# Kernel optimization log

Measured on AMD Instinct MI355X. Metric: run time of the kernel, lower is better.

Reference implementation:

```python
import jax, jax.numpy as jnp
import numpy as np

N, D, E = 50000, 128, 800000


def setup_inputs() -> dict:
    key = jax.random.key(0)
    ks = jax.random.split(key, 12)
    s = 1.0 / np.sqrt(D)
    return {
        "x": jax.random.normal(ks[0], (N, D), jnp.float32),
        "edge_index": jax.random.randint(ks[1], (2, E), 0, N, jnp.int32),
        "W1": jax.random.normal(ks[2], (D, D), jnp.float32) * s,
        "bc1": jnp.zeros((D,), jnp.float32),
        "W2": jax.random.normal(ks[3], (D, D), jnp.float32) * s,
        "bc2": jnp.zeros((D,), jnp.float32),
        "w11": jax.random.normal(ks[4], (D, D), jnp.float32) * s,
        "w12": jax.random.normal(ks[5], (D, D), jnp.float32) * s,
        "b1": jax.random.uniform(ks[6], (D,), jnp.float32, -s, s),
        "w21": jax.random.normal(ks[7], (D, D), jnp.float32) * s,
        "w22": jax.random.normal(ks[8], (D, D), jnp.float32) * s,
        "b2": jax.random.uniform(ks[9], (D,), jnp.float32, -s, s),
    }


def gcn_conv(x, W, b, src, dst):
    """PyG GCNConv: self-loops + symmetric D^-1/2 (A+I) D^-1/2 normalization."""
    n = x.shape[0]
    h = x @ W  # [N, D]
    ones = jnp.ones(dst.shape[0], h.dtype)
    deg = jax.ops.segment_sum(ones, dst, num_segments=n) + 1.0  # +1 for self-loop
    dinv = jax.lax.rsqrt(deg)
    norm = dinv[src] * dinv[dst]  # [E]
    agg = jax.ops.segment_sum(h[src] * norm[:, None], dst, num_segments=n)
    agg = agg + h * (dinv * dinv)[:, None]  # self-loop messages
    return agg + b


def reference(x, edge_index, W1, bc1, W2, bc2, w11, w12, b1, w21, w22, b2):
    src, dst = edge_index[0], edge_index[1]
    # layer 1: forward and reversed edge directions (dropout is identity in eval)
    o1 = jax.nn.relu(gcn_conv(x, W1, bc1, src, dst))
    o2 = jax.nn.relu(gcn_conv(x, W1, bc1, dst, src))
    G = jax.nn.sigmoid(o1 @ w11.T + o2 @ w12.T + b1)
    h = G * o1 + (1.0 - G) * o2
    # layer 2
    p1 = jax.nn.relu(gcn_conv(h, W2, bc2, src, dst))
    p2 = jax.nn.relu(gcn_conv(h, W2, bc2, dst, src))
    G2 = jax.nn.sigmoid(p1 @ w21.T + p2 @ w22.T + b2)
    return G2 * p1 + (1.0 - G2) * p2
```

## Files before the change

kernel.cpp:

```cpp
#include <hip/hip_runtime.h>
#include <hip/hip_bf16.h>
#include <hip/hip_fp16.h>
#include <math.h>

#define D 128
#define SEG 4096
#define BSH 7
#define RCAP 4096
#define ACAP 4096
#define TRS 133

typedef _Float16 half8  __attribute__((ext_vector_type(8)));
typedef _Float16 half4v __attribute__((ext_vector_type(4)));
typedef float    fx4    __attribute__((ext_vector_type(4)));

__global__ __launch_bounds__(256) void scat2_kernel(const int* __restrict__ src,
                                                    const int* __restrict__ dst,
                                                    int e, int nb,
                                                    int* __restrict__ gcur1, int* __restrict__ gcur2,
                                                    unsigned int* __restrict__ rec1,
                                                    unsigned int* __restrict__ rec2) {
    __shared__ int h1[512], h2[512], o1[512], o2[512], run1[512], run2[512];
    int tid = threadIdx.x;
    for (int b = tid; b < nb; b += 256) { h1[b] = 0; h2[b] = 0; run1[b] = 0; run2[b] = 0; }
    __syncthreads();
    int s0 = blockIdx.x * SEG;
    int s1 = min(e, s0 + SEG);
    for (int idx = s0 + tid; idx < s1; idx += 256) {
        atomicAdd(&h1[dst[idx] >> BSH], 1);
        atomicAdd(&h2[src[idx] >> BSH], 1);
    }
    __syncthreads();
    for (int b = tid; b < nb; b += 256) {
        o1[b] = atomicAdd(&gcur1[b], h1[b]);
        o2[b] = atomicAdd(&gcur2[b], h2[b]);
    }
    __syncthreads();
    for (int idx = s0 + tid; idx < s1; idx += 256) {
        unsigned int sv = (unsigned int)src[idx];
        unsigned int dv = (unsigned int)dst[idx];
        int b1 = dv >> BSH, b2 = sv >> BSH;
        int p1 = o1[b1] + atomicAdd(&run1[b1], 1);
        if (p1 < RCAP) rec1[(size_t)b1 * RCAP + p1] = (dv << 16) | sv;
        int p2 = o2[b2] + atomicAdd(&run2[b2], 1);
        if (p2 < RCAP) rec2[(size_t)b2 * RCAP + p2] = (sv << 16) | dv;
    }
}

__global__ __launch_bounds__(256) void fin_kernel(const unsigned int* __restrict__ rec1,
                                                  const unsigned int* __restrict__ rec2,
                                                  const int* __restrict__ gcur1, const int* __restrict__ gcur2,
                                                  unsigned short* __restrict__ adj1, unsigned short* __restrict__ adj2,
                                                  int* __restrict__ ip1, int* __restrict__ ipe1,
                                                  int* __restrict__ ip2, int* __restrict__ ipe2,
                                                  float* __restrict__ dinv1, float* __restrict__ dinv2,
                                                  int n) {
    __shared__ unsigned int Lrec[RCAP];
    __shared__ unsigned short sadj[ACAP];
    __shared__ int deg[128], pscan[128], cur[128];
    __shared__ int ptot_s;
    int bkt = blockIdx.x;
    int dir = blockIdx.y;
    const unsigned int* rec = dir ? rec2 : rec1;
    const int* gc = dir ? gcur2 : gcur1;
    unsigned short* adj = dir ? adj2 : adj1;
    int* ip  = dir ? ip2 : ip1;
    int* ipe = dir ? ipe2 : ipe1;
    float* dinv = dir ? dinv2 : dinv1;

    int tid = threadIdx.x;
    int cnt = gc[bkt];
    if (cnt > RCAP) cnt = RCAP;
    size_t rbase = (size_t)bkt * RCAP;
    if (tid < 128) { deg[tid] = 0; cur[tid] = 0; }
    for (int i = tid; i < cnt; i += 256) Lrec[i] = rec[rbase + i];
    __syncthreads();
    int base = bkt << BSH;
    for (int i = tid; i < cnt; i += 256)
        atomicAdd(&deg[(int)(Lrec[i] >> 16) - base], 1);
    __syncthreads();
    if (tid < 128) pscan[tid] = (deg[tid] + 7) & ~7;
    __syncthreads();
    #pragma unroll
    for (int st = 1; st < 128; st <<= 1) {
        int add = (tid < 128 && tid >= st) ? pscan[tid - st] : 0;
        __syncthreads();
        if (tid < 128) pscan[tid] += add;
        __syncthreads();
    }
    if (tid == 127) ptot_s = min(pscan[127], ACAP);
    __syncthreads();
    int ptot = ptot_s;
    for (int i = tid; i < ptot; i += 256) sadj[i] = (unsigned short)n;
    __syncthreads();
    for (int i = tid; i < cnt; i += 256) {
        unsigned int r = Lrec[i];
        int l = (int)(r >> 16) - base;
        int pd = (deg[l] + 7) & ~7;
        int pos = pscan[l] - pd + atomicAdd(&cur[l], 1);
        if (pos < ACAP) sadj[pos] = (unsigned short)(r & 0xffffu);
    }
    __syncthreads();
    int gbase = bkt * ACAP;
    for (int i = tid; i < ptot; i += 256) adj[gbase + i] = sadj[i];
    if (tid < 128) {
        int node = base + tid;
        if (node < n) {
            int pd = (deg[tid] + 7) & ~7;
            ip[node]  = gbase + pscan[tid] - pd;
            ipe[node] = gbase + pscan[tid];
            dinv[node] = rsqrtf((float)deg[tid] + 1.0f);
        }
    }
    if (bkt == 0 && tid == 200) dinv[n] = 0.0f;
}

__global__ __launch_bounds__(256) void prep_kernel(const float* __restrict__ W1, const float* __restrict__ W2,
                                                   const float* __restrict__ w11, const float* __restrict__ w12,
                                                   const float* __restrict__ w21, const float* __restrict__ w22,
                                                   _Float16* __restrict__ T1, _Float16* __restrict__ T2,
                                                   _Float16* __restrict__ o11, _Float16* __restrict__ o12,
                                                   _Float16* __restrict__ o21, _Float16* __restrict__ o22) {
    __shared__ float s[32][33];
    int which = blockIdx.y;
    if (which < 2) {
        const float* w = which ? W2 : W1;
        _Float16* t = which ? T2 : T1;
        int tk = (blockIdx.x >> 2) * 32;
        int tc = (blockIdx.x & 3) * 32;
        int lr = threadIdx.x >> 5;
        int lc = threadIdx.x & 31;
        #pragma unroll
        for (int i = 0; i < 32; i += 8)
            s[lr + i][lc] = w[(size_t)(tk + lr + i) * D + tc + lc];
        __syncthreads();
        #pragma unroll
        for (int i = 0; i < 32; i += 8)
            t[(size_t)(tc + lr + i) * D + tk + lc] = (_Float16)s[lc][lr + i];
    } else {
        int wsel = which - 2;
        const float* w = (wsel == 0) ? w11 : (wsel == 1) ? w12 : (wsel == 2) ? w21 : w22;
        _Float16* o = (wsel == 0) ? o11 : (wsel == 1) ? o12 : (wsel == 2) ? o21 : o22;
        int idx = (blockIdx.x * 256 + threadIdx.x) * 4;
        float4 v = *(const float4*)&w[idx];
        half4v h = {(_Float16)v.x, (_Float16)v.y, (_Float16)v.z, (_Float16)v.w};
        *(half4v*)&o[idx] = h;
    }
}

__global__ __launch_bounds__(256) void gemm_f32a_kernel(const float* __restrict__ A,
                                                        const _Float16* __restrict__ Wt,
                                                        _Float16* __restrict__ C16, int n) {
    __shared__ float trs[4][16 * TRS];
    int tid = threadIdx.x;
    int wv = tid >> 6, lane = tid & 63;
    int m = lane & 15, q = lane >> 4;
    int row0 = blockIdx.x * 128 + wv * 32;
    size_t ar0 = (size_t)min(row0 + m, n - 1) * D;
    size_t ar1 = (size_t)min(row0 + 16 + m, n - 1) * D;
    fx4 acc[2][8];
    #pragma unroll
    for (int t = 0; t < 2; t++)
        #pragma unroll
        for (int ct = 0; ct < 8; ct++) acc[t][ct] = (fx4){0.f, 0.f, 0.f, 0.f};
    #pragma unroll
    for (int ks = 0; ks < 4; ks++) {
        int k0 = ks * 32 + q * 8;
        half8 bf[8];
        #pragma unroll
        for (int ct = 0; ct < 8; ct++)
            bf[ct] = *(const half8*)&Wt[(size_t)(ct * 16 + m) * D + k0];
        float4 u0 = *(const float4*)&A[ar0 + k0];
        float4 u1 = *(const float4*)&A[ar0 + k0 + 4];
        half8 a0 = {(_Float16)u0.x, (_Float16)u0.y, (_Float16)u0.z, (_Float16)u0.w,
                    (_Float16)u1.x, (_Float16)u1.y, (_Float16)u1.z, (_Float16)u1.w};
        float4 v0 = *(const float4*)&A[ar1 + k0];
        float4 v1 = *(const float4*)&A[ar1 + k0 + 4];
        half8 a1 = {(_Float16)v0.x, (_Float16)v0.y, (_Float16)v0.z, (_Float16)v0.w,
                    (_Float16)v1.x, (_Float16)v1.y, (_Float16)v1.z, (_Float16)v1.w};
        #pragma unroll
        for (int ct = 0; ct < 8; ct++) {
            acc[0][ct] = __builtin_amdgcn_mfma_f32_16x16x32_f16(a0, bf[ct], acc[0][ct], 0, 0, 0);
            acc[1][ct] = __builtin_amdgcn_mfma_f32_16x16x32_f16(a1, bf[ct], acc[1][ct], 0, 0, 0);
        }
    }
    float* Wl = trs[wv];
    #pragma unroll
    for (int t = 0; t < 2; t++) {
        #pragma unroll
        for (int reg = 0; reg < 4; reg++)
            #pragma unroll
            for (int ct = 0; ct < 8; ct++)
                Wl[(q * 4 + reg) * TRS + ct * 16 + m] = acc[t][ct][reg];
        int r = row0 + t * 16 + m;
        if (r < n) {
            size_t rr = (size_t)r * D;
            #pragma unroll
            for (int ks = 0; ks < 4; ks++) {
                int c0 = ks * 32 + q * 8;
                float4 p0 = *(const float4*)&Wl[m * TRS + c0];
                float4 p1 = *(const float4*)&Wl[m * TRS + c0 + 4];
                half8 hv = {(_Float16)p0.x, (_Float16)p0.y, (_Float16)p0.z, (_Float16)p0.w,
                            (_Float16)p1.x, (_Float16)p1.y, (_Float16)p1.z, (_Float16)p1.w};
                *(half8*)&C16[rr + c0] = hv;
            }
        }
    }
}

__global__ __launch_bounds__(256) void gemm_f16a_kernel(const _Float16* __restrict__ A,
                                                        const _Float16* __restrict__ Wt,
                                                        _Float16* __restrict__ C16, int n) {
    __shared__ float trs[4][16 * TRS];
    int tid = threadIdx.x;
    int wv = tid >> 6, lane = tid & 63;
    int m = lane & 15, q = lane >> 4;
    int row0 = blockIdx.x * 128 + wv * 32;
    size_t ar0 = (size_t)min(row0 + m, n - 1) * D;
    size_t ar1 = (size_t)min(row0 + 16 + m, n - 1) * D;
    fx4 acc[2][8];
    #pragma unroll
    for (int t = 0; t < 2; t++)
        #pragma unroll
        for (int ct = 0; ct < 8; ct++) acc[t][ct] = (fx4){0.f, 0.f, 0.f, 0.f};
    #pragma unroll
    for (int ks = 0; ks < 4; ks++) {
        int k0 = ks * 32 + q * 8;
        half8 bf[8];
        #pragma unroll
        for (int ct = 0; ct < 8; ct++)
            bf[ct] = *(const half8*)&Wt[(size_t)(ct * 16 + m) * D + k0];
        half8 a0 = *(const half8*)&A[ar0 + k0];
        half8 a1 = *(const half8*)&A[ar1 + k0];
        #pragma unroll
        for (int ct = 0; ct < 8; ct++) {
            acc[0][ct] = __builtin_amdgcn_mfma_f32_16x16x32_f16(a0, bf[ct], acc[0][ct], 0, 0, 0);
            acc[1][ct] = __builtin_amdgcn_mfma_f32_16x16x32_f16(a1, bf[ct], acc[1][ct], 0, 0, 0);
        }
    }
    float* Wl = trs[wv];
    #pragma unroll
    for (int t = 0; t < 2; t++) {
        #pragma unroll
        for (int reg = 0; reg < 4; reg++)
            #pragma unroll
            for (int ct = 0; ct < 8; ct++)
                Wl[(q * 4 + reg) * TRS + ct * 16 + m] = acc[t][ct][reg];
        int r = row0 + t * 16 + m;
        if (r < n) {
            size_t rr = (size_t)r * D;
            #pragma unroll
            for (int ks = 0; ks < 4; ks++) {
                int c0 = ks * 32 + q * 8;
                float4 p0 = *(const float4*)&Wl[m * TRS + c0];
                float4 p1 = *(const float4*)&Wl[m * TRS + c0 + 4];
                half8 hv = {(_Float16)p0.x, (_Float16)p0.y, (_Float16)p0.z, (_Float16)p0.w,
                            (_Float16)p1.x, (_Float16)p1.y, (_Float16)p1.z, (_Float16)p1.w};
                *(half8*)&C16[rr + c0] = hv;
            }
        }
    }
}

__global__ __launch_bounds__(256) void aggregate2_kernel(const __half* __restrict__ h16,
                                                         const int* __restrict__ ip1,
                                                         const int* __restrict__ ipe1,
                                                         const unsigned short* __restrict__ adj1,
                                                         const float* __restrict__ dinv1,
                                                         const int* __restrict__ ip2,
                                                         const int* __restrict__ ipe2,
                                                         const unsigned short* __restrict__ adj2,
                                                         const float* __restrict__ dinv2,
                                                         const float* __restrict__ bias,
                                                         _Float16* __restrict__ out1,
                                                         _Float16* __restrict__ out2, int n) {
    const int* ip  = blockIdx.y ? ip2 : ip1;
    const int* ipe = blockIdx.y ? ipe2 : ipe1;
    const unsigned short* adj = blockIdx.y ? adj2 : adj1;
    const float* dinv = blockIdx.y ? dinv2 : dinv1;
    _Float16* out = blockIdx.y ? out2 : out1;
    int wid = threadIdx.x >> 6, lane = threadIdx.x & 63;
    int half = lane >> 5, l32 = lane & 31;
    int i = blockIdx.x * 4 + wid;
    if (i >= n) return;
    int beg = ip[i], endp = ipe[i];
    int sh = half * 16;
    float4 acc = make_float4(0.f, 0.f, 0.f, 0.f);
    for (int j = beg; j < endp; j += 8) {
        uint4 av = *(const uint4*)&adj[j];
        int s0 = (av.x >> sh) & 0xffff;
        int s1 = (av.y >> sh) & 0xffff;
        int s2 = (av.z >> sh) & 0xffff;
        int s3 = (av.w >> sh) & 0xffff;
        float w0 = dinv[s0], w1 = dinv[s1], w2 = dinv[s2], w3 = dinv[s3];
        uint2 r0 = *(const uint2*)&h16[(size_t)s0 * D + 4 * l32];
        uint2 r1 = *(const uint2*)&h16[(size_t)s1 * D + 4 * l32];
        uint2 r2 = *(const uint2*)&h16[(size_t)s2 * D + 4 * l32];
        uint2 r3 = *(const uint2*)&h16[(size_t)s3 * D + 4 * l32];
        float2 a0 = __half22float2(*(__half2*)&r0.x), b0 = __half22float2(*(__half2*)&r0.y);
        float2 a1 = __half22float2(*(__half2*)&r1.x), b1 = __half22float2(*(__half2*)&r1.y);
        float2 a2 = __half22float2(*(__half2*)&r2.x), b2 = __half22float2(*(__half2*)&r2.y);
        float2 a3 = __half22float2(*(__half2*)&r3.x), b3 = __half22float2(*(__half2*)&r3.y);
        acc.x += w0 * a0.x + w1 * a1.x + w2 * a2.x + w3 * a3.x;
        acc.y += w0 * a0.y + w1 * a1.y + w2 * a2.y + w3 * a3.y;
        acc.z += w0 * b0.x + w1 * b1.x + w2 * b2.x + w3 * b3.x;
        acc.w += w0 * b0.y + w1 * b1.y + w2 * b2.y + w3 * b3.y;
    }
    acc.x += __shfl_xor(acc.x, 32, 64);
    acc.y += __shfl_xor(acc.y, 32, 64);
    acc.z += __shfl_xor(acc.z, 32, 64);
    acc.w += __shfl_xor(acc.w, 32, 64);
    if (half == 0) {
        float di = dinv[i];
        float d2 = di * di;
        uint2 rs = *(const uint2*)&h16[(size_t)i * D + 4 * l32];
        float2 s0 = __half22float2(*(__half2*)&rs.x);
        float2 s1 = __half22float2(*(__half2*)&rs.y);
        float4 bv = *(const float4*)&bias[4 * l32];
        half4v o;
        o[0] = (_Float16)fmaxf(di * acc.x + d2 * s0.x + bv.x, 0.f);
        o[1] = (_Float16)fmaxf(di * acc.y + d2 * s0.y + bv.y, 0.f);
        o[2] = (_Float16)fmaxf(di * acc.z + d2 * s1.x + bv.z, 0.f);
        o[3] = (_Float16)fmaxf(di * acc.w + d2 * s1.y + bv.w, 0.f);
        *(half4v*)&out[(size_t)i * D + 4 * l32] = o;
    }
}

__global__ __launch_bounds__(256) void gate_mfma_kernel(const _Float16* __restrict__ o1,
                                                        const _Float16* __restrict__ o2,
                                                        const _Float16* __restrict__ w1,
                                                        const _Float16* __restrict__ w2,
                                                        const float* __restrict__ b,
                                                        float* __restrict__ out32,
                                                        _Float16* __restrict__ out16,
                                                        int write16, int n) {
    __shared__ float trs[4][16 * TRS];
    int tid = threadIdx.x;
    int wv = tid >> 6, lane = tid & 63;
    int m = lane & 15, q = lane >> 4;
    int row0 = blockIdx.x * 128 + wv * 32;
    size_t ar0 = (size_t)min(row0 + m, n - 1) * D;
    size_t ar1 = (size_t)min(row0 + 16 + m, n - 1) * D;
    fx4 acc[2][8];
    #pragma unroll
    for (int t = 0; t < 2; t++)
        #pragma unroll
        for (int ct = 0; ct < 8; ct++) acc[t][ct] = (fx4){0.f, 0.f, 0.f, 0.f};
    #pragma unroll
    for (int ks = 0; ks < 4; ks++) {
        int k0 = ks * 32 + q * 8;
        half8 bf1[8], bf2[8];
        #pragma unroll
        for (int ct = 0; ct < 8; ct++) {
            bf1[ct] = *(const half8*)&w1[(size_t)(ct * 16 + m) * D + k0];
            bf2[ct] = *(const half8*)&w2[(size_t)(ct * 16 + m) * D + k0];
        }
        half8 a10 = *(const half8*)&o1[ar0 + k0];
        half8 a20 = *(const half8*)&o2[ar0 + k0];
        half8 a11 = *(const half8*)&o1[ar1 + k0];
        half8 a21 = *(const half8*)&o2[ar1 + k0];
        #pragma unroll
        for (int ct = 0; ct < 8; ct++) {
            acc[0][ct] = __builtin_amdgcn_mfma_f32_16x16x32_f16(a10, bf1[ct], acc[0][ct], 0, 0, 0);
            acc[0][ct] = __builtin_amdgcn_mfma_f32_16x16x32_f16(a20, bf2[ct], acc[0][ct], 0, 0, 0);
            acc[1][ct] = __builtin_amdgcn_mfma_f32_16x16x32_f16(a11, bf1[ct], acc[1][ct], 0, 0, 0);
            acc[1][ct] = __builtin_amdgcn_mfma_f32_16x16x32_f16(a21, bf2[ct], acc[1][ct], 0, 0, 0);
        }
    }
    float bb[4][8];
    #pragma unroll
    for (int ks = 0; ks < 4; ks++) {
        float4 b0 = *(const float4*)&b[ks * 32 + q * 8];
        float4 b1 = *(const float4*)&b[ks * 32 + q * 8 + 4];
        bb[ks][0] = b0.x; bb[ks][1] = b0.y; bb[ks][2] = b0.z; bb[ks][3] = b0.w;
        bb[ks][4] = b1.x; bb[ks][5] = b1.y; bb[ks][6] = b1.z; bb[ks][7] = b1.w;
    }
    float* Wl = trs[wv];
    #pragma unroll
    for (int t = 0; t < 2; t++) {
        #pragma unroll
        for (int reg = 0; reg < 4; reg++)
            #pragma unroll
            for (int ct = 0; ct < 8; ct++)
                Wl[(q * 4 + reg) * TRS + ct * 16 + m] = acc[t][ct][reg];
        int r = row0 + t * 16 + m;
        size_t rr = (size_t)min(r, n - 1) * D;
        #pragma unroll
        for (int ks = 0; ks < 4; ks++) {
            int c0 = ks * 32 + q * 8;
            float4 p0 = *(const float4*)&Wl[m * TRS + c0];
            float4 p1 = *(const float4*)&Wl[m * TRS + c0 + 4];
            half8 u1 = *(const half8*)&o1[rr + c0];
            half8 u2 = *(const half8*)&o2[rr + c0];
            float pv[8] = {p0.x, p0.y, p0.z, p0.w, p1.x, p1.y, p1.z, p1.w};
            float res[8];
            #pragma unroll
            for (int j = 0; j < 8; j++) {
                float tv = pv[j] + bb[ks][j];
                float g = 1.0f / (1.0f + __expf(-tv));
                res[j] = g * (float)u1[j] + (1.0f - g) * (float)u2[j];
            }
            if (r < n) {
                if (write16) {
                    half8 hv = {(_Float16)res[0], (_Float16)res[1], (_Float16)res[2], (_Float16)res[3],
                                (_Float16)res[4], (_Float16)res[5], (_Float16)res[6], (_Float16)res[7]};
                    *(half8*)&out16[rr + c0] = hv;
                } else {
                    *(float4*)&out32[rr + c0]     = make_float4(res[0], res[1], res[2], res[3]);
                    *(float4*)&out32[rr + c0 + 4] = make_float4(res[4], res[5], res[6], res[7]);
                }
            }
        }
    }
}

extern "C" void kernel_launch(void* const* d_in, const int* in_sizes, int n_in,
                              void* d_out, int out_size, void* d_ws, size_t ws_size,
                              hipStream_t stream) {
    const float* x   = (const float*)d_in[0];
    const int*   eix = (const int*)d_in[1];
    const float* W1  = (const float*)d_in[2];
    const float* bc1 = (const float*)d_in[3];
    const float* W2  = (const float*)d_in[4];
    const float* bc2 = (const float*)d_in[5];
    const float* w11 = (const float*)d_in[6];
    const float* w12 = (const float*)d_in[7];
    const float* b1  = (const float*)d_in[8];
    const float* w21 = (const float*)d_in[9];
    const float* w22 = (const float*)d_in[10];
    const float* b2  = (const float*)d_in[11];
    int n = in_sizes[0] / D;
    int e = in_sizes[1] / 2;
    const int* src = eix;
    const int* dst = eix + e;

    int nb = (n + 127) >> BSH;
    int nblk = (e + SEG - 1) / SEG;

    char* p = (char*)d_ws;
    auto alloc = [&](size_t bytes) {
        char* q = p;
        p += (bytes + 255) & ~(size_t)255;
        return q;
    };
    int* gcur1 = (int*)alloc((size_t)2 * 512 * sizeof(int));
    int* gcur2 = gcur1 + 512;
    unsigned int* rec1 = (unsigned int*)alloc((size_t)nb * RCAP * sizeof(unsigned int));
    unsigned int* rec2 = (unsigned int*)alloc((size_t)nb * RCAP * sizeof(unsigned int));
    int*   ip1   = (int*)alloc((size_t)n * sizeof(int));
    int*   ipe1  = (int*)alloc((size_t)n * sizeof(int));
    int*   ip2   = (int*)alloc((size_t)n * sizeof(int));
    int*   ipe2  = (int*)alloc((size_t)n * sizeof(int));
    float* dinv1 = (float*)alloc((size_t)(n + 1) * sizeof(float));
    float* dinv2 = (float*)alloc((size_t)(n + 1) * sizeof(float));
    unsigned short* adj1 = (unsigned short*)alloc((size_t)nb * ACAP * sizeof(unsigned short));
    unsigned short* adj2 = (unsigned short*)alloc((size_t)nb * ACAP * sizeof(unsigned short));
    _Float16* W1t  = (_Float16*)alloc((size_t)D * D * sizeof(_Float16));
    _Float16* W2t  = (_Float16*)alloc((size_t)D * D * sizeof(_Float16));
    _Float16* w11h = (_Float16*)alloc((size_t)D * D * sizeof(_Float16));
    _Float16* w12h = (_Float16*)alloc((size_t)D * D * sizeof(_Float16));
    _Float16* w21h = (_Float16*)alloc((size_t)D * D * sizeof(_Float16));
    _Float16* w22h = (_Float16*)alloc((size_t)D * D * sizeof(_Float16));
    _Float16* h16  = (_Float16*)alloc((size_t)(n + 1) * D * sizeof(_Float16));
    _Float16* o1h  = (_Float16*)alloc((size_t)n * D * sizeof(_Float16));
    _Float16* o2h  = (_Float16*)alloc((size_t)n * D * sizeof(_Float16));
    _Float16* h2h  = (_Float16*)alloc((size_t)n * D * sizeof(_Float16));
    float* outF  = (float*)d_out;

    hipMemsetAsync(gcur1, 0, (size_t)2 * 512 * sizeof(int), stream);
    prep_kernel<<<dim3(16, 6), 256, 0, stream>>>(W1, W2, w11, w12, w21, w22,
                                                 W1t, W2t, w11h, w12h, w21h, w22h);
    scat2_kernel<<<nblk, 256, 0, stream>>>(src, dst, e, nb, gcur1, gcur2, rec1, rec2);
    fin_kernel<<<dim3(nb, 2), 256, 0, stream>>>(rec1, rec2, gcur1, gcur2,
                                                adj1, adj2, ip1, ipe1, ip2, ipe2, dinv1, dinv2, n);

    int gG = (n + 127) / 128;
    int gA = (n + 3) / 4;
    gemm_f32a_kernel<<<gG, 256, 0, stream>>>(x, W1t, h16, n);
    aggregate2_kernel<<<dim3(gA, 2), 256, 0, stream>>>((const __half*)h16,
                                                       ip1, ipe1, adj1, dinv1,
                                                       ip2, ipe2, adj2, dinv2,
                                                       bc1, o1h, o2h, n);
    gate_mfma_kernel<<<gG, 256, 0, stream>>>(o1h, o2h, w11h, w12h, b1,
                                             nullptr, h2h, 1, n);
    gemm_f16a_kernel<<<gG, 256, 0, stream>>>(h2h, W2t, h16, n);
    aggregate2_kernel<<<dim3(gA, 2), 256, 0, stream>>>((const __half*)h16,
                                                       ip1, ipe1, adj1, dinv1,
                                                       ip2, ipe2, adj2, dinv2,
                                                       bc2, o1h, o2h, n);
    gate_mfma_kernel<<<gG, 256, 0, stream>>>(o1h, o2h, w21h, w22h, b2,
                                             outF, nullptr, 0, n);
}
```

Baseline: 330.6 us.

## Pre-scale GEMM outputs by source dinv to drop per-edge degree gathers

The GEMM epilogues now write two fp16 copies of h, each pre-multiplied by the per-node dinv of one edge direction. This lets the aggregation kernel skip the per-edge dinv gather and multiply, and fold the self-loop term as di*(acc + hs[i]). The aggregate loop also prefetches the next adjacency chunk, uses a 32-bit index calculation, and splits the epilogue across both half-waves. The cost is double the GEMM write traffic and an extra N×D fp16 buffer, and the padding row is now zeroed by memset instead of through dinv[n]=0.

```diff
diff --git a/kernel.cpp b/kernel.cpp
--- a/kernel.cpp
+++ b/kernel.cpp
@@ -112,7 +112,6 @@
             dinv[node] = rsqrtf((float)deg[tid] + 1.0f);
         }
     }
-    if (bkt == 0 && tid == 200) dinv[n] = 0.0f;
 }
 
 __global__ __launch_bounds__(256) void prep_kernel(const float* __restrict__ W1, const float* __restrict__ W2,
@@ -150,7 +149,10 @@
 
 __global__ __launch_bounds__(256) void gemm_f32a_kernel(const float* __restrict__ A,
                                                         const _Float16* __restrict__ Wt,
-                                                        _Float16* __restrict__ C16, int n) {
+                                                        const float* __restrict__ dinv1,
+                                                        const float* __restrict__ dinv2,
+                                                        _Float16* __restrict__ hs1,
+                                                        _Float16* __restrict__ hs2, int n) {
     __shared__ float trs[4][16 * TRS];
     int tid = threadIdx.x;
     int wv = tid >> 6, lane = tid & 63;
@@ -194,15 +196,22 @@
                 Wl[(q * 4 + reg) * TRS + ct * 16 + m] = acc[t][ct][reg];
         int r = row0 + t * 16 + m;
         if (r < n) {
+            float s1 = dinv1[r], s2 = dinv2[r];
             size_t rr = (size_t)r * D;
             #pragma unroll
             for (int ks = 0; ks < 4; ks++) {
                 int c0 = ks * 32 + q * 8;
                 float4 p0 = *(const float4*)&Wl[m * TRS + c0];
                 float4 p1 = *(const float4*)&Wl[m * TRS + c0 + 4];
-                half8 hv = {(_Float16)p0.x, (_Float16)p0.y, (_Float16)p0.z, (_Float16)p0.w,
-                            (_Float16)p1.x, (_Float16)p1.y, (_Float16)p1.z, (_Float16)p1.w};
-                *(half8*)&C16[rr + c0] = hv;
+                float pv[8] = {p0.x, p0.y, p0.z, p0.w, p1.x, p1.y, p1.z, p1.w};
+                half8 h1v, h2v;
+                #pragma unroll
+                for (int j = 0; j < 8; j++) {
+                    h1v[j] = (_Float16)(s1 * pv[j]);
+                    h2v[j] = (_Float16)(s2 * pv[j]);
+                }
+                *(half8*)&hs1[rr + c0] = h1v;
+                *(half8*)&hs2[rr + c0] = h2v;
             }
         }
     }
@@ -210,7 +219,10 @@
 
 __global__ __launch_bounds__(256) void gemm_f16a_kernel(const _Float16* __restrict__ A,
                                                         const _Float16* __restrict__ Wt,
-                                                        _Float16* __restrict__ C16, int n) {
+                                                        const float* __restrict__ dinv1,
+                                                        const float* __restrict__ dinv2,
+                                                        _Float16* __restrict__ hs1,
+                                                        _Float16* __restrict__ hs2, int n) {
     __shared__ float trs[4][16 * TRS];
     int tid = threadIdx.x;
     int wv = tid >> 6, lane = tid & 63;
@@ -248,21 +260,29 @@
                 Wl[(q * 4 + reg) * TRS + ct * 16 + m] = acc[t][ct][reg];
         int r = row0 + t * 16 + m;
         if (r < n) {
+            float s1 = dinv1[r], s2 = dinv2[r];
             size_t rr = (size_t)r * D;
             #pragma unroll
             for (int ks = 0; ks < 4; ks++) {
                 int c0 = ks * 32 + q * 8;
                 float4 p0 = *(const float4*)&Wl[m * TRS + c0];
                 float4 p1 = *(const float4*)&Wl[m * TRS + c0 + 4];
-                half8 hv = {(_Float16)p0.x, (_Float16)p0.y, (_Float16)p0.z, (_Float16)p0.w,
-                            (_Float16)p1.x, (_Float16)p1.y, (_Float16)p1.z, (_Float16)p1.w};
-                *(half8*)&C16[rr + c0] = hv;
+                float pv[8] = {p0.x, p0.y, p0.z, p0.w, p1.x, p1.y, p1.z, p1.w};
+                half8 h1v, h2v;
+                #pragma unroll
+                for (int j = 0; j < 8; j++) {
+                    h1v[j] = (_Float16)(s1 * pv[j]);
+                    h2v[j] = (_Float16)(s2 * pv[j]);
+                }
+                *(half8*)&hs1[rr + c0] = h1v;
+                *(half8*)&hs2[rr + c0] = h2v;
             }
         }
     }
 }
 
-__global__ __launch_bounds__(256) void aggregate2_kernel(const __half* __restrict__ h16,
+__global__ __launch_bounds__(256) void aggregate2_kernel(const __half* __restrict__ hs1g,
+                                                         const __half* __restrict__ hs2g,
                                                          const int* __restrict__ ip1,
                                                          const int* __restrict__ ipe1,
                                                          const unsigned short* __restrict__ adj1,
@@ -274,56 +294,60 @@
                                                          const float* __restrict__ bias,
                                                          _Float16* __restrict__ out1,
                                                          _Float16* __restrict__ out2, int n) {
+    const __half* hs = blockIdx.y ? hs2g : hs1g;
     const int* ip  = blockIdx.y ? ip2 : ip1;
     const int* ipe = blockIdx.y ? ipe2 : ipe1;
     const unsigned short* adj = blockIdx.y ? adj2 : adj1;
     const float* dinv = blockIdx.y ? dinv2 : dinv1;
     _Float16* out = blockIdx.y ? out2 : out1;
     int wid = threadIdx.x >> 6, lane = threadIdx.x & 63;
-    int half = lane >> 5, l32 = lane & 31;
+    int hf = lane >> 5, l32 = lane & 31;
     int i = blockIdx.x * 4 + wid;
     if (i >= n) return;
     int beg = ip[i], endp = ipe[i];
-    int sh = half * 16;
+    int fcol = 4 * l32;
     float4 acc = make_float4(0.f, 0.f, 0.f, 0.f);
-    for (int j = beg; j < endp; j += 8) {
-        uint4 av = *(const uint4*)&adj[j];
-        int s0 = (av.x >> sh) & 0xffff;
-        int s1 = (av.y >> sh) & 0xffff;
-        int s2 = (av.z >> sh) & 0xffff;
-        int s3 = (av.w >> sh) & 0xffff;
-        float w0 = dinv[s0], w1 = dinv[s1], w2 = dinv[s2], w3 = dinv[s3];
-        uint2 r0 = *(const uint2*)&h16[(size_t)s0 * D + 4 * l32];
-        uint2 r1 = *(const uint2*)&h16[(size_t)s1 * D + 4 * l32];
-        uint2 r2 = *(const uint2*)&h16[(size_t)s2 * D + 4 * l32];
-        uint2 r3 = *(const uint2*)&h16[(size_t)s3 * D + 4 * l32];
-        float2 a0 = __half22float2(*(__half2*)&r0.x), b0 = __half22float2(*(__half2*)&r0.y);
-        float2 a1 = __half22float2(*(__half2*)&r1.x), b1 = __half22float2(*(__half2*)&r1.y);
-        float2 a2 = __half22float2(*(__half2*)&r2.x), b2 = __half22float2(*(__half2*)&r2.y);
-        float2 a3 = __half22float2(*(__half2*)&r3.x), b3 = __half22float2(*(__half2*)&r3.y);
-        acc.x += w0 * a0.x + w1 * a1.x + w2 * a2.x + w3 * a3.x;
-        acc.y += w0 * a0.y + w1 * a1.y + w2 * a2.y + w3 * a3.y;
-        acc.z += w0 * b0.x + w1 * b1.x + w2 * b2.x + w3 * b3.x;
-        acc.w += w0 * b0.y + w1 * b1.y + w2 * b2.y + w3 * b3.y;
+    if (beg < endp) {
+        int hoff = hf << 2;
+        int j = beg;
+        uint2 iv = *(const uint2*)&adj[j + hoff];
+        while (true) {
+            int jn = j + 8;
+            int jp = jn < endp ? jn : j;
+            uint2 niv = *(const uint2*)&adj[jp + hoff];
+            int s0 = iv.x & 0xffff, s1 = iv.x >> 16;
+            int s2 = iv.y & 0xffff, s3 = iv.y >> 16;
+            uint2 r0 = *(const uint2*)&hs[(s0 << 7) + fcol];
+            uint2 r1 = *(const uint2*)&hs[(s1 << 7) + fcol];
+            uint2 r2 = *(const uint2*)&hs[(s2 << 7) + fcol];
+            uint2 r3 = *(const uint2*)&hs[(s3 << 7) + fcol];
+            float2 a0 = __half22float2(*(__half2*)&r0.x), b0 = __half22float2(*(__half2*)&r0.y);
+            float2 a1 = __half22float2(*(__half2*)&r1.x), b1 = __half22float2(*(__half2*)&r1.y);
+            float2 a2 = __half22float2(*(__half2*)&r2.x), b2 = __half22float2(*(__half2*)&r2.y);
+            float2 a3 = __half22float2(*(__half2*)&r3.x), b3 = __half22float2(*(__half2*)&r3.y);
+            acc.x += a0.x + a1.x + a2.x + a3.x;
+            acc.y += a0.y + a1.y + a2.y + a3.y;
+            acc.z += b0.x + b1.x + b2.x + b3.x;
+            acc.w += b0.y + b1.y + b2.y + b3.y;
+            if (jn >= endp) break;
+            iv = niv; j = jn;
+        }
     }
     acc.x += __shfl_xor(acc.x, 32, 64);
     acc.y += __shfl_xor(acc.y, 32, 64);
     acc.z += __shfl_xor(acc.z, 32, 64);
     acc.w += __shfl_xor(acc.w, 32, 64);
-    if (half == 0) {
-        float di = dinv[i];
-        float d2 = di * di;
-        uint2 rs = *(const uint2*)&h16[(size_t)i * D + 4 * l32];
-        float2 s0 = __half22float2(*(__half2*)&rs.x);
-        float2 s1 = __half22float2(*(__half2*)&rs.y);
-        float4 bv = *(const float4*)&bias[4 * l32];
-        half4v o;
-        o[0] = (_Float16)fmaxf(di * acc.x + d2 * s0.x + bv.x, 0.f);
-        o[1] = (_Float16)fmaxf(di * acc.y + d2 * s0.y + bv.y, 0.f);
-        o[2] = (_Float16)fmaxf(di * acc.z + d2 * s1.x + bv.z, 0.f);
-        o[3] = (_Float16)fmaxf(di * acc.w + d2 * s1.y + bv.w, 0.f);
-        *(half4v*)&out[(size_t)i * D + 4 * l32] = o;
-    }
+    float di = dinv[i];
+    float ax = hf ? acc.z : acc.x;
+    float ay = hf ? acc.w : acc.y;
+    int off = (i << 7) + fcol + 2 * hf;
+    unsigned int rs = *(const unsigned int*)&hs[off];
+    float2 sv = __half22float2(*(const __half2*)&rs);
+    float2 bv = *(const float2*)&bias[fcol + 2 * hf];
+    float r0f = fmaxf(di * (ax + sv.x) + bv.x, 0.f);
+    float r1f = fmaxf(di * (ay + sv.y) + bv.y, 0.f);
+    __half2 hv = __floats2half2_rn(r0f, r1f);
+    *(__half2*)&out[off] = hv;
 }
 
 __global__ __launch_bounds__(256) void gate_mfma_kernel(const _Float16* __restrict__ o1,
@@ -461,13 +485,16 @@
     _Float16* w12h = (_Float16*)alloc((size_t)D * D * sizeof(_Float16));
     _Float16* w21h = (_Float16*)alloc((size_t)D * D * sizeof(_Float16));
     _Float16* w22h = (_Float16*)alloc((size_t)D * D * sizeof(_Float16));
-    _Float16* h16  = (_Float16*)alloc((size_t)(n + 1) * D * sizeof(_Float16));
+    _Float16* hs1  = (_Float16*)alloc((size_t)(n + 1) * D * sizeof(_Float16));
+    _Float16* hs2  = (_Float16*)alloc((size_t)(n + 1) * D * sizeof(_Float16));
     _Float16* o1h  = (_Float16*)alloc((size_t)n * D * sizeof(_Float16));
     _Float16* o2h  = (_Float16*)alloc((size_t)n * D * sizeof(_Float16));
     _Float16* h2h  = (_Float16*)alloc((size_t)n * D * sizeof(_Float16));
     float* outF  = (float*)d_out;
 
     hipMemsetAsync(gcur1, 0, (size_t)2 * 512 * sizeof(int), stream);
+    hipMemsetAsync(hs1 + (size_t)n * D, 0, D * sizeof(_Float16), stream);
+    hipMemsetAsync(hs2 + (size_t)n * D, 0, D * sizeof(_Float16), stream);
     prep_kernel<<<dim3(16, 6), 256, 0, stream>>>(W1, W2, w11, w12, w21, w22,
                                                  W1t, W2t, w11h, w12h, w21h, w22h);
     scat2_kernel<<<nblk, 256, 0, stream>>>(src, dst, e, nb, gcur1, gcur2, rec1, rec2);
@@ -476,18 +503,17 @@
 
     int gG = (n + 127) / 128;
     int gA = (n + 3) / 4;
-    gemm_f32a_kernel<<<gG, 256, 0, stream>>>(x, W1t, h16, n);
-    aggregate2_kernel<<<dim3(gA, 2), 256, 0, stream>>>((const __half*)h16,
+    gemm_f32a_kernel<<<gG, 256, 0, stream>>>(x, W1t, dinv1, dinv2, hs1, hs2, n);
+    aggregate2_kernel<<<dim3(gA, 2), 256, 0, stream>>>((const __half*)hs1, (const __half*)hs2,
                                                        ip1, ipe1, adj1, dinv1,
                                                        ip2, ipe2, adj2, dinv2,
                                                        bc1, o1h, o2h, n);
     gate_mfma_kernel<<<gG, 256, 0, stream>>>(o1h, o2h, w11h, w12h, b1,
                                              nullptr, h2h, 1, n);
-    gemm_f16a_kernel<<<gG, 256, 0, stream>>>(h2h, W2t, h16, n);
-    aggregate2_kernel<<<dim3(gA, 2), 256, 0, stream>>>((const __half*)h16,
+    gemm_f16a_kernel<<<gG, 256, 0, stream>>>(h2h, W2t, dinv1, dinv2, hs1, hs2, n);
+    aggregate2_kernel<<<dim3(gA, 2), 256, 0, stream>>>((const __half*)hs1, (const __half*)hs2,
                                                        ip1, ipe1, adj1, dinv1,
                                                        ip2, ipe2, adj2, dinv2,
                                                        bc2, o1h, o2h, n);
-    gate_mfma_kernel<<<gG, 256, 0, stream>>>(o1h, o2h, w21h, w22h, b2,
-                                             outF, nullptr, 0, n);
-}
+    gate_mfma_kernel<<<gG, 256, 0, stream>>>(o1h, o2h, w21h, w22h, b2, outF, nullptr, 0, n);
+}
```

Measured after the change: 331.8 us. About the same (+0.4%).
